# Kernel optimization log

Hardware: AMD Instinct MI355X
Metric: run time of the kernel (lower is better)

Reference implementation:

```python
import jax, jax.numpy as jnp
import numpy as np

N, E = 50000, 600000
IN_DIM, H, D = 256, 4, 128
NEG_SLOPE = 0.2


def setup_inputs() -> dict:
    key = jax.random.key(0)
    ks = jax.random.split(key, 9)
    x = jax.random.normal(ks[0], (N, IN_DIM), dtype=jnp.float32)
    src = jax.random.randint(ks[1], (E,), 0, N, dtype=jnp.int32)
    dst = jax.random.randint(ks[2], (E,), 0, N, dtype=jnp.int32)
    # layer 0: in=256 -> H*D=512; layer 1: in=H*D=512 -> H*D=512
    s0 = 1.0 / np.sqrt(IN_DIM)
    s1 = 1.0 / np.sqrt(H * D)
    W0 = jax.random.normal(ks[3], (IN_DIM, H * D), dtype=jnp.float32) * s0
    al0 = jax.random.normal(ks[4], (H, D), dtype=jnp.float32) * s1
    ar0 = jax.random.normal(ks[5], (H, D), dtype=jnp.float32) * s1
    W1 = jax.random.normal(ks[6], (H * D, H * D), dtype=jnp.float32) * s1
    al1 = jax.random.normal(ks[7], (H, D), dtype=jnp.float32) * s1
    ar1 = jax.random.normal(ks[8], (H, D), dtype=jnp.float32) * s1
    return {"x": x, "src": src, "dst": dst,
            "W0": W0, "al0": al0, "ar0": ar0,
            "W1": W1, "al1": al1, "ar1": ar1}


def gat_conv(x, W, al, ar, src, dst):
    """One DGL-style GATConv layer. x:[N,in] -> out:[N,H,D] (post relu)."""
    h = (x @ W).reshape(N, H, D)                       # fc, no bias
    el = jnp.sum(h * al, axis=-1)                      # [N,H]
    er = jnp.sum(h * ar, axis=-1)                      # [N,H]
    e = jax.nn.leaky_relu(el[src] + er[dst], NEG_SLOPE)  # [E,H]
    # edge softmax over incoming edges of each dst node (numerically stable)
    m = jax.ops.segment_max(e, dst, num_segments=N)    # [N,H]
    m = jnp.where(jnp.isfinite(m), m, 0.0)             # empty segments -> -inf
    ex = jnp.exp(e - m[dst])                           # [E,H]
    denom = jax.ops.segment_sum(ex, dst, num_segments=N)  # [N,H]
    alpha = ex / denom[dst]                            # [E,H]
    msg = alpha[:, :, None] * h[src]                   # [E,H,D]
    rst = jax.ops.segment_sum(msg, dst, num_segments=N)  # [N,H,D]
    return jax.nn.relu(rst)                            # activation=F.relu


def reference(x, src, dst, W0, al0, ar0, W1, al1, ar1):
    h = gat_conv(x, W0, al0, ar0, src, dst)            # [N,H,D]
    h = h.reshape(N, H * D)                            # flatten(1)
    h = gat_conv(h, W1, al1, ar1, src, dst)            # [N,H,D]
    return h.mean(axis=1)                              # mean over heads -> [N,D]
```

## Files before the change

kernel.cpp:

```cpp
#include <hip/hip_runtime.h>

#define NN 50000
#define NE 600000
#define DD 128
#define HD 512
#define NB 196

typedef unsigned short u16;
typedef __attribute__((ext_vector_type(8))) short short8;
typedef __attribute__((ext_vector_type(4))) float floatx4;

__device__ inline float b2f(u16 u) {
  return __uint_as_float(((unsigned int)u) << 16);
}
__device__ inline u16 f2b(float f) {
  unsigned int u = __float_as_uint(f);
  u = u + 0x7FFFu + ((u >> 16) & 1u);
  return (u16)(u >> 16);
}

__device__ inline void load_lds16(const u16* g, u16* l) {
  __builtin_amdgcn_global_load_lds(
      (const __attribute__((address_space(1))) unsigned int*)(uintptr_t)g,
      (__attribute__((address_space(3))) unsigned int*)(uintptr_t)l,
      16, 0, 0);
}

__global__ void zero_k(int* __restrict__ p, int n) {
  int i = blockIdx.x * 256 + threadIdx.x;
  if (i < n) p[i] = 0;
}

__global__ void transpose_k(const float* __restrict__ W, u16* __restrict__ Wt, int K) {
  int idx = blockIdx.x * 256 + threadIdx.x;
  if (idx >= K * 512) return;
  int k = idx >> 9, n = idx & 511;
  Wt[n * K + k] = f2b(W[idx]);
}

__global__ void count_k(const int* __restrict__ dst, int* __restrict__ counts) {
  int e = blockIdx.x * 256 + threadIdx.x;
  if (e < NE) atomicAdd(&counts[dst[e]], 1);
}

__global__ __launch_bounds__(256) void blockscan_k(const int* __restrict__ counts,
                                                   int* __restrict__ rowp,
                                                   int* __restrict__ bsums) {
  __shared__ int tmp[256];
  int t = threadIdx.x;
  int i = blockIdx.x * 256 + t;
  int v = (i < NN) ? counts[i] : 0;
  tmp[t] = v;
  __syncthreads();
  for (int off = 1; off < 256; off <<= 1) {
    int u = (t >= off) ? tmp[t - off] : 0;
    __syncthreads();
    tmp[t] += u;
    __syncthreads();
  }
  if (i < NN) rowp[i] = tmp[t] - v;
  if (t == 255) bsums[blockIdx.x] = tmp[t];
}

__global__ __launch_bounds__(256) void bscan_k(const int* __restrict__ bsums,
                                               int* __restrict__ boffs) {
  __shared__ int tmp[256];
  int t = threadIdx.x;
  int v = (t < NB) ? bsums[t] : 0;
  tmp[t] = v;
  __syncthreads();
  for (int off = 1; off < 256; off <<= 1) {
    int u = (t >= off) ? tmp[t - off] : 0;
    __syncthreads();
    tmp[t] += u;
    __syncthreads();
  }
  if (t < NB) boffs[t] = tmp[t] - v;
}

__global__ void addoff_k(int* __restrict__ rowp, int* __restrict__ cursor,
                         const int* __restrict__ boffs) {
  int i = blockIdx.x * 256 + threadIdx.x;
  if (i < NN) {
    int v = rowp[i] + boffs[blockIdx.x];
    rowp[i] = v;
    cursor[i] = v;
  }
  if (i == 0) rowp[NN] = NE;
}

__global__ void scatter_k(const int* __restrict__ src, const int* __restrict__ dst,
                          int* __restrict__ cursor, int* __restrict__ csrs) {
  int e = blockIdx.x * 256 + threadIdx.x;
  if (e < NE) {
    int d = dst[e];
    int pos = atomicAdd(&cursor[d], 1);
    csrs[pos] = src[e];
  }
}

template <int K, bool A_F32>
__global__ __launch_bounds__(512) void gemm_el_er(
    const void* __restrict__ Ap, const u16* __restrict__ Wt,
    const float* __restrict__ al, const float* __restrict__ ar,
    u16* __restrict__ h, float* __restrict__ el, float* __restrict__ er) {
  __shared__ u16 Wt_s[512 * 32];

  const int tid = threadIdx.x;
  const int w = tid >> 6, lane = tid & 63, quad = lane >> 4, l16 = lane & 15;
  const int rg = w >> 1, cg = w & 1;
  const int bm = blockIdx.x;

  floatx4 acc[16] = {};

  const int rowA = bm * 64 + rg * 16 + l16;
  const long arow = (rowA < NN) ? rowA : (NN - 1);

  const int drow = lane >> 2;
  const int q8 = ((lane & 3) ^ ((lane >> 3) & 3)) * 8;
  const int p4 = (quad ^ ((l16 >> 1) & 3)) * 8;

  for (int k0 = 0; k0 < K; k0 += 32) {
#pragma unroll
    for (int rr = 0; rr < 4; ++rr) {
      const int rbase = rr * 128 + w * 16;
      load_lds16(Wt + (long)(rbase + drow) * K + k0 + q8, Wt_s + rbase * 32);
    }
    short8 af;
    if (A_F32) {
      const float* Af = (const float*)Ap;
      floatx4 v0 = *(const floatx4*)(Af + arow * K + k0 + quad * 8);
      floatx4 v1 = *(const floatx4*)(Af + arow * K + k0 + quad * 8 + 4);
      u16 tmp[8];
#pragma unroll
      for (int j = 0; j < 4; ++j) tmp[j] = f2b(v0[j]);
#pragma unroll
      for (int j = 0; j < 4; ++j) tmp[4 + j] = f2b(v1[j]);
      af = *(short8*)tmp;
    } else {
      af = *(const short8*)((const u16*)Ap + arow * K + k0 + quad * 8);
    }
    __syncthreads();
#pragma unroll
    for (int ct = 0; ct < 16; ++ct) {
      short8 bf = *(const short8*)(Wt_s + (cg * 256 + ct * 16 + l16) * 32 + p4);
      acc[ct] = __builtin_amdgcn_mfma_f32_16x16x32_bf16(af, bf, acc[ct], 0, 0, 0);
    }
    __syncthreads();
  }

  float alv[16], arv[16];
#pragma unroll
  for (int ct = 0; ct < 16; ++ct) {
    int col = cg * 256 + ct * 16 + l16;
    alv[ct] = al[col];
    arv[ct] = ar[col];
  }
#pragma unroll
  for (int reg = 0; reg < 4; ++reg) {
    const int r = bm * 64 + rg * 16 + quad * 4 + reg;
    float pel[2] = {0.f, 0.f}, per_[2] = {0.f, 0.f};
#pragma unroll
    for (int ct = 0; ct < 16; ++ct) {
      int hh = ct >> 3;
      float v = acc[ct][reg];
      pel[hh] += v * alv[ct];
      per_[hh] += v * arv[ct];
    }
#pragma unroll
    for (int m = 1; m < 16; m <<= 1) {
      pel[0] += __shfl_xor(pel[0], m, 64);
      pel[1] += __shfl_xor(pel[1], m, 64);
      per_[0] += __shfl_xor(per_[0], m, 64);
      per_[1] += __shfl_xor(per_[1], m, 64);
    }
    if (r < NN) {
#pragma unroll
      for (int ct = 0; ct < 16; ++ct)
        h[(long)r * HD + cg * 256 + ct * 16 + l16] = f2b(acc[ct][reg]);
      if (l16 == 0) {
        el[r * 4 + cg * 2] = pel[0];
        el[r * 4 + cg * 2 + 1] = pel[1];
        er[r * 4 + cg * 2] = per_[0];
        er[r * 4 + cg * 2 + 1] = per_[1];
      }
    }
  }
}

template <int MODE>
__global__ __launch_bounds__(256) void aggregate(
    const u16* __restrict__ h, const float* __restrict__ el,
    const float* __restrict__ er, const int* __restrict__ rowp,
    const int* __restrict__ csrs, u16* __restrict__ ob, float* __restrict__ of) {
  const int wv = threadIdx.x >> 6, lane = threadIdx.x & 63;
  const int n = blockIdx.x * 4 + wv;
  if (n >= NN) return;
  const int base = rowp[n];
  const int deg = rowp[n + 1] - base;
  const int head = lane >> 4;

  if (deg == 0) {
    if (MODE == 0) {
      short8 z = {};
      *(short8*)(ob + (long)n * HD + lane * 8) = z;
    } else if (lane < 16) {
      floatx4 z = {};
      *(floatx4*)(of + (long)n * DD + lane * 8) = z;
      *(floatx4*)(of + (long)n * DD + lane * 8 + 4) = z;
    }
    return;
  }

  const float er_h = er[n * 4 + head];

  float acc[8] = {0.f, 0.f, 0.f, 0.f, 0.f, 0.f, 0.f, 0.f};
  float sm = 0.f;
  int i = 0;
  for (; i + 4 <= deg; i += 4) {
    int s0 = csrs[base + i], s1 = csrs[base + i + 1];
    int s2 = csrs[base + i + 2], s3 = csrs[base + i + 3];
    const short8 hv0 = *(const short8*)(h + (long)s0 * HD + lane * 8);
    const short8 hv1 = *(const short8*)(h + (long)s1 * HD + lane * 8);
    const short8 hv2 = *(const short8*)(h + (long)s2 * HD + lane * 8);
    const short8 hv3 = *(const short8*)(h + (long)s3 * HD + lane * 8);
    float e0 = el[s0 * 4 + head] + er_h;
    float e1 = el[s1 * 4 + head] + er_h;
    float e2 = el[s2 * 4 + head] + er_h;
    float e3 = el[s3 * 4 + head] + er_h;
    e0 = (e0 > 0.f) ? e0 : 0.2f * e0;
    e1 = (e1 > 0.f) ? e1 : 0.2f * e1;
    e2 = (e2 > 0.f) ? e2 : 0.2f * e2;
    e3 = (e3 > 0.f) ? e3 : 0.2f * e3;
    float w0 = __expf(e0);
    float w1 = __expf(e1);
    float w2 = __expf(e2);
    float w3 = __expf(e3);
    sm += (w0 + w1) + (w2 + w3);
#pragma unroll
    for (int j = 0; j < 8; ++j) acc[j] += w0 * b2f((u16)hv0[j]);
#pragma unroll
    for (int j = 0; j < 8; ++j) acc[j] += w1 * b2f((u16)hv1[j]);
#pragma unroll
    for (int j = 0; j < 8; ++j) acc[j] += w2 * b2f((u16)hv2[j]);
#pragma unroll
    for (int j = 0; j < 8; ++j) acc[j] += w3 * b2f((u16)hv3[j]);
  }
  for (; i < deg; ++i) {
    int s = csrs[base + i];
    float e = el[s * 4 + head] + er_h;
    const short8 hv = *(const short8*)(h + (long)s * HD + lane * 8);
    e = (e > 0.f) ? e : 0.2f * e;
    float wgt = __expf(e);
    sm += wgt;
#pragma unroll
    for (int j = 0; j < 8; ++j) acc[j] += wgt * b2f((u16)hv[j]);
  }

  const float inv = 1.f / sm;
#pragma unroll
  for (int j = 0; j < 8; ++j) acc[j] = fmaxf(acc[j] * inv, 0.f);

  if (MODE == 0) {
    u16 ub[8];
#pragma unroll
    for (int j = 0; j < 8; ++j) ub[j] = f2b(acc[j]);
    *(short8*)(ob + (long)n * HD + lane * 8) = *(short8*)ub;
  } else {
#pragma unroll
    for (int j = 0; j < 8; ++j) acc[j] += __shfl_xor(acc[j], 16, 64);
#pragma unroll
    for (int j = 0; j < 8; ++j) acc[j] += __shfl_xor(acc[j], 32, 64);
    if (lane < 16) {
      floatx4 o0, o1;
#pragma unroll
      for (int j = 0; j < 4; ++j) o0[j] = acc[j] * 0.25f;
#pragma unroll
      for (int j = 0; j < 4; ++j) o1[j] = acc[4 + j] * 0.25f;
      *(floatx4*)(of + (long)n * DD + lane * 8) = o0;
      *(floatx4*)(of + (long)n * DD + lane * 8 + 4) = o1;
    }
  }
}

extern "C" void kernel_launch(void* const* d_in, const int* in_sizes, int n_in,
                              void* d_out, int out_size, void* d_ws, size_t ws_size,
                              hipStream_t stream) {
  const float* x = (const float*)d_in[0];
  const int* src = (const int*)d_in[1];
  const int* dst = (const int*)d_in[2];
  const float* W0 = (const float*)d_in[3];
  const float* al0 = (const float*)d_in[4];
  const float* ar0 = (const float*)d_in[5];
  const float* W1 = (const float*)d_in[6];
  const float* al1 = (const float*)d_in[7];
  const float* ar1 = (const float*)d_in[8];
  float* out = (float*)d_out;

  char* p = (char*)d_ws;
  u16* h = (u16*)p;        p += (size_t)NN * HD * 2;
  u16* rst0 = (u16*)p;     p += (size_t)NN * HD * 2;
  float* el = (float*)p;   p += (size_t)NN * 4 * 4;
  float* er = (float*)p;   p += (size_t)NN * 4 * 4;
  u16* Wt0 = (u16*)p;      p += 512 * 256 * 2;
  u16* Wt1 = (u16*)p;      p += 512 * 512 * 2;
  int* counts = (int*)p;   p += (size_t)NN * 4;
  int* cursor = (int*)p;   p += (size_t)NN * 4;
  int* rowp = (int*)p;     p += (size_t)(NN + 1) * 4;
  int* bsums = (int*)p;    p += 256 * 4;
  int* boffs = (int*)p;    p += 256 * 4;
  int* csrs = (int*)p;     p += (size_t)NE * 4;

  zero_k<<<NB, 256, 0, stream>>>(counts, NN);
  count_k<<<(NE + 255) / 256, 256, 0, stream>>>(dst, counts);
  blockscan_k<<<NB, 256, 0, stream>>>(counts, rowp, bsums);
  bscan_k<<<1, 256, 0, stream>>>(bsums, boffs);
  addoff_k<<<NB, 256, 0, stream>>>(rowp, cursor, boffs);
  scatter_k<<<(NE + 255) / 256, 256, 0, stream>>>(src, dst, cursor, csrs);
  transpose_k<<<(256 * 512 + 255) / 256, 256, 0, stream>>>(W0, Wt0, 256);
  transpose_k<<<(512 * 512 + 255) / 256, 256, 0, stream>>>(W1, Wt1, 512);

  const int gblocks = (NN + 63) / 64;
  gemm_el_er<256, true><<<gblocks, 512, 0, stream>>>(x, Wt0, al0, ar0, h, el, er);
  aggregate<0><<<(NN + 3) / 4, 256, 0, stream>>>(h, el, er, rowp, csrs, rst0, nullptr);
  gemm_el_er<512, false><<<gblocks, 512, 0, stream>>>(rst0, Wt1, al1, ar1, h, el, er);
  aggregate<1><<<(NN + 3) / 4, 256, 0, stream>>>(h, el, er, rowp, csrs, nullptr, out);
}
```

Baseline: 462.7 us.

## Compute edge softmax weights cooperatively per lane and batch neighbor gathers by eight

Each lane of the wave now handles one incoming edge at a time, up to 64 per chunk. It loads the source index and all four heads' el values, computes the leaky-relu exp weights and stages them in LDS. Before, every lane redundantly reloaded the index and el for each edge. The gather loop then broadcasts source indices with readlane and issues eight row loads in flight, and the four per-head softmax sums are reduced with xor shuffles at the end. The last batch may load up to seven padded rows, using the clamped index, with zero weight, which wastes some bandwidth for low-degree nodes. Output stores also become nontemporal.

```diff
diff --git a/kernel.cpp b/kernel.cpp
--- a/kernel.cpp
+++ b/kernel.cpp
@@ -193,6 +193,7 @@
     const u16* __restrict__ h, const float* __restrict__ el,
     const float* __restrict__ er, const int* __restrict__ rowp,
     const int* __restrict__ csrs, u16* __restrict__ ob, float* __restrict__ of) {
+  __shared__ float w_s[4][64][4];
   const int wv = threadIdx.x >> 6, lane = threadIdx.x & 63;
   const int n = blockIdx.x * 4 + wv;
   if (n >= NN) return;
@@ -203,59 +204,63 @@
   if (deg == 0) {
     if (MODE == 0) {
       short8 z = {};
-      *(short8*)(ob + (long)n * HD + lane * 8) = z;
+      __builtin_nontemporal_store(z, (short8*)(ob + (long)n * HD + lane * 8));
     } else if (lane < 16) {
       floatx4 z = {};
-      *(floatx4*)(of + (long)n * DD + lane * 8) = z;
-      *(floatx4*)(of + (long)n * DD + lane * 8 + 4) = z;
+      __builtin_nontemporal_store(z, (floatx4*)(of + (long)n * DD + lane * 8));
+      __builtin_nontemporal_store(z, (floatx4*)(of + (long)n * DD + lane * 8 + 4));
     }
     return;
   }
 
-  const float er_h = er[n * 4 + head];
+  const floatx4 er4 = *(const floatx4*)(er + n * 4);
 
   float acc[8] = {0.f, 0.f, 0.f, 0.f, 0.f, 0.f, 0.f, 0.f};
-  float sm = 0.f;
-  int i = 0;
-  for (; i + 4 <= deg; i += 4) {
-    int s0 = csrs[base + i], s1 = csrs[base + i + 1];
-    int s2 = csrs[base + i + 2], s3 = csrs[base + i + 3];
-    const short8 hv0 = *(const short8*)(h + (long)s0 * HD + lane * 8);
-    const short8 hv1 = *(const short8*)(h + (long)s1 * HD + lane * 8);
-    const short8 hv2 = *(const short8*)(h + (long)s2 * HD + lane * 8);
-    const short8 hv3 = *(const short8*)(h + (long)s3 * HD + lane * 8);
-    float e0 = el[s0 * 4 + head] + er_h;
-    float e1 = el[s1 * 4 + head] + er_h;
-    float e2 = el[s2 * 4 + head] + er_h;
-    float e3 = el[s3 * 4 + head] + er_h;
-    e0 = (e0 > 0.f) ? e0 : 0.2f * e0;
-    e1 = (e1 > 0.f) ? e1 : 0.2f * e1;
-    e2 = (e2 > 0.f) ? e2 : 0.2f * e2;
-    e3 = (e3 > 0.f) ? e3 : 0.2f * e3;
-    float w0 = __expf(e0);
-    float w1 = __expf(e1);
-    float w2 = __expf(e2);
-    float w3 = __expf(e3);
-    sm += (w0 + w1) + (w2 + w3);
-#pragma unroll
-    for (int j = 0; j < 8; ++j) acc[j] += w0 * b2f((u16)hv0[j]);
-#pragma unroll
-    for (int j = 0; j < 8; ++j) acc[j] += w1 * b2f((u16)hv1[j]);
-#pragma unroll
-    for (int j = 0; j < 8; ++j) acc[j] += w2 * b2f((u16)hv2[j]);
-#pragma unroll
-    for (int j = 0; j < 8; ++j) acc[j] += w3 * b2f((u16)hv3[j]);
-  }
-  for (; i < deg; ++i) {
-    int s = csrs[base + i];
-    float e = el[s * 4 + head] + er_h;
-    const short8 hv = *(const short8*)(h + (long)s * HD + lane * 8);
-    e = (e > 0.f) ? e : 0.2f * e;
-    float wgt = __expf(e);
-    sm += wgt;
-#pragma unroll
-    for (int j = 0; j < 8; ++j) acc[j] += wgt * b2f((u16)hv[j]);
-  }
+  float sm0 = 0.f, sm1 = 0.f, sm2 = 0.f, sm3 = 0.f;
+
+  for (int c0 = 0; c0 < deg; c0 += 64) {
+    const int cnt = min(deg - c0, 64);
+
+    const int l = c0 + lane;
+    const int idx = csrs[base + ((l < deg) ? l : (deg - 1))];
+    const floatx4 el4 = *(const floatx4*)(el + (long)idx * 4);
+    floatx4 w4;
+#pragma unroll
+    for (int j = 0; j < 4; ++j) {
+      float e = el4[j] + er4[j];
+      e = (e > 0.f) ? e : 0.2f * e;
+      w4[j] = (l < deg) ? __expf(e) : 0.f;
+    }
+    sm0 += w4[0];
+    sm1 += w4[1];
+    sm2 += w4[2];
+    sm3 += w4[3];
+    *(floatx4*)(&w_s[wv][lane][0]) = w4;
+
+    for (int i = 0; i < cnt; i += 8) {
+      short8 hv[8];
+#pragma unroll
+      for (int u = 0; u < 8; ++u) {
+        const int s = __builtin_amdgcn_readlane(idx, i + u);
+        hv[u] = *(const short8*)(h + (long)s * HD + lane * 8);
+      }
+#pragma unroll
+      for (int u = 0; u < 8; ++u) {
+        const float w = w_s[wv][i + u][head];
+#pragma unroll
+        for (int j = 0; j < 8; ++j) acc[j] += w * b2f((u16)hv[u][j]);
+      }
+    }
+  }
+
+#pragma unroll
+  for (int m = 1; m < 64; m <<= 1) {
+    sm0 += __shfl_xor(sm0, m, 64);
+    sm1 += __shfl_xor(sm1, m, 64);
+    sm2 += __shfl_xor(sm2, m, 64);
+    sm3 += __shfl_xor(sm3, m, 64);
+  }
+  const float sm = (head == 0) ? sm0 : (head == 1) ? sm1 : (head == 2) ? sm2 : sm3;
 
   const float inv = 1.f / sm;
 #pragma unroll
@@ -265,7 +270,7 @@
     u16 ub[8];
 #pragma unroll
     for (int j = 0; j < 8; ++j) ub[j] = f2b(acc[j]);
-    *(short8*)(ob + (long)n * HD + lane * 8) = *(short8*)ub;
+    __builtin_nontemporal_store(*(short8*)ub, (short8*)(ob + (long)n * HD + lane * 8));
   } else {
 #pragma unroll
     for (int j = 0; j < 8; ++j) acc[j] += __shfl_xor(acc[j], 16, 64);
@@ -277,8 +282,8 @@
       for (int j = 0; j < 4; ++j) o0[j] = acc[j] * 0.25f;
 #pragma unroll
       for (int j = 0; j < 4; ++j) o1[j] = acc[4 + j] * 0.25f;
-      *(floatx4*)(of + (long)n * DD + lane * 8) = o0;
-      *(floatx4*)(of + (long)n * DD + lane * 8 + 4) = o1;
+      __builtin_nontemporal_store(o0, (floatx4*)(of + (long)n * DD + lane * 8));
+      __builtin_nontemporal_store(o1, (floatx4*)(of + (long)n * DD + lane * 8 + 4));
     }
   }
 }
```

New measurement: 475.2 us. 1.03x slower.
